# Performance work log

Measured on AMD Instinct MI355X. Metric: run time of the kernel, lower is better.

The kernel has to match this reference:

```python
import jax, jax.numpy as jnp
import numpy as np

B, T, S, D = 8, 512, 512, 1024
NUM_HEADS = 16
REUSE_HEADS = 8
NEW_HEADS = NUM_HEADS - REUSE_HEADS
KEY_DIM = 64
VALUE_DIM = 64
PE_MAX = 512  # pe_max_seq_length


def setup_inputs() -> dict:
    key = jax.random.key(0)
    ks = jax.random.split(key, 12)
    s = 0.02
    return {
        "query": jax.random.normal(ks[0], (B, T, D), jnp.float32),
        "value": jax.random.normal(ks[1], (B, S, D), jnp.float32),
        # scores reused from a previous layer (already softmaxed there)
        "reuse_attention_scores": jax.random.uniform(ks[2], (B, REUSE_HEADS, T, S), jnp.float32),
        "Wq": jax.random.normal(ks[3], (D, NEW_HEADS, KEY_DIM), jnp.float32) * s,
        "bq": jnp.zeros((NEW_HEADS, KEY_DIM), jnp.float32),
        "Wk": jax.random.normal(ks[4], (D, NEW_HEADS, KEY_DIM), jnp.float32) * s,
        "bk": jnp.zeros((NEW_HEADS, KEY_DIM), jnp.float32),
        "Wv": jax.random.normal(ks[5], (D, NUM_HEADS, VALUE_DIM), jnp.float32) * s,
        "bv": jnp.zeros((NUM_HEADS, VALUE_DIM), jnp.float32),
        # relative position embeddings: [1, new_heads, 2*PE_MAX - 1]
        "pos_emb": jax.random.truncated_normal(ks[6], -2.0, 2.0, (1, NEW_HEADS, 2 * PE_MAX - 1), jnp.float32) * 0.2,
        # output denses: one for reused heads (no bias), one for new heads (bias)
        "Wo_reuse": jax.random.normal(ks[7], (REUSE_HEADS, VALUE_DIM, D), jnp.float32) * s,
        "Wo_new": jax.random.normal(ks[8], (NEW_HEADS, VALUE_DIM, D), jnp.float32) * s,
        "bo": jnp.zeros((D,), jnp.float32),
    }


def reference(query, value, reuse_attention_scores, Wq, bq, Wk, bk, Wv, bv,
              pos_emb, Wo_reuse, Wo_new, bo):
    # projections (EinsumDense abc,cde->abde + bias over last two dims)
    q = jnp.einsum("btd,dnh->btnh", query, Wq) + bq           # [B,T,Hn,kd]
    k = jnp.einsum("bsd,dnh->bsnh", value, Wk) + bk           # [B,S,Hn,kd]
    v = jnp.einsum("bsd,dnh->bsnh", value, Wv) + bv           # [B,S,H,vd]
    v_reuse, v_new = v[:, :, :REUSE_HEADS, :], v[:, :, REUSE_HEADS:, :]

    # new-head scores: scaled QK^T  (dot_product_equation 'aecd,abcd->acbe')
    q = q * (1.0 / np.sqrt(float(KEY_DIM)))
    new_scores = jnp.einsum("bsnh,btnh->bnts", k, q)          # [B,Hn,T,S]

    # relative position bias: index = clip(key_pos - query_pos + PE_MAX-1)
    rel = jnp.arange(S)[None, :] - jnp.arange(T)[:, None] + (PE_MAX - 1)
    rel = jnp.clip(rel, 0, 2 * PE_MAX - 2)                    # [T,S]
    bias = pos_emb[0][:, rel]                                 # [Hn,T,S]
    new_scores = jax.nn.softmax(new_scores + bias[None], axis=-1)

    # reused heads consume previous-layer scores directly (dropout=0)
    reuse_scores = reuse_attention_scores[:, :REUSE_HEADS]
    out_reuse = jnp.einsum("bnts,bsnh->btnh", reuse_scores, v_reuse)
    out_new = jnp.einsum("bnts,bsnh->btnh", new_scores, v_new)

    # separate output projections, summed; bias only on the new-heads dense
    out = (jnp.einsum("btnh,nhd->btd", out_reuse, Wo_reuse)
           + jnp.einsum("btnh,nhd->btd", out_new, Wo_new) + bo)
    return out
```

## Files before the change

### kernel.cpp

```cpp
#include <hip/hip_runtime.h>
#include <hip/hip_bf16.h>

typedef __bf16 bf16_t;
typedef __bf16 bf16x8 __attribute__((ext_vector_type(8)));
typedef float  f32x4  __attribute__((ext_vector_type(4)));

#define GLDS(gsrc, ldst)                                                              \
  __builtin_amdgcn_global_load_lds(                                                   \
      (const __attribute__((address_space(1))) unsigned int*)(gsrc),                  \
      (__attribute__((address_space(3))) unsigned int*)(ldst), 16, 0, 0)

__global__ void k_convert2(const float* __restrict__ a, bf16_t* __restrict__ da,
                           const float* __restrict__ b, bf16_t* __restrict__ db, int n8) {
  int i = blockIdx.x * blockDim.x + threadIdx.x;
  const float* s; bf16_t* d;
  if (i < n8) { s = a; d = da; } else { s = b; d = db; i -= n8; }
  const float4* p = reinterpret_cast<const float4*>(s) + 2 * (long)i;
  float4 x = p[0], y = p[1];
  bf16x8 o;
  o[0] = (bf16_t)x.x; o[1] = (bf16_t)x.y; o[2] = (bf16_t)x.z; o[3] = (bf16_t)x.w;
  o[4] = (bf16_t)y.x; o[5] = (bf16_t)y.y; o[6] = (bf16_t)y.z; o[7] = (bf16_t)y.w;
  reinterpret_cast<bf16x8*>(d)[i] = o;
}

struct TArgs {
  const float* src[5];
  bf16_t* dst[5];
  int C[5], Ct[5], off[5], blk0[6];
  float scale[5];
};
__global__ void k_transpose5(TArgs ta) {
  __shared__ float tile[32][33];
  const int bid = blockIdx.x;
  int s = 0;
  while (bid >= ta.blk0[s + 1]) ++s;
  const int bi = bid - ta.blk0[s];
  const int Ct = ta.Ct[s];
  const int c0 = (bi % Ct) * 32, r0 = (bi / Ct) * 32;
  const int C = ta.C[s];
  const float* src = ta.src[s];
  const int lx = threadIdx.x & 31, ly = threadIdx.x >> 5;
  #pragma unroll
  for (int i = 0; i < 32; i += 8)
    tile[ly + i][lx] = src[(long)(r0 + ly + i) * C + (c0 + lx)];
  __syncthreads();
  const float sc = ta.scale[s];
  bf16_t* dst = ta.dst[s];
  const int off = ta.off[s];
  #pragma unroll
  for (int i = 0; i < 32; i += 8)
    dst[(long)(c0 + ly + i) * 1024 + off + (r0 + lx)] = (bf16_t)(tile[lx][ly + i] * sc);
}

struct ProjItem {
  const bf16_t* A; const bf16_t* B; bf16_t* C; const float* bias;
  float bscale; int ldc; int writeT;
};
struct ProjArgs { ProjItem it[3]; };

__global__ __launch_bounds__(256)
void k_gemm_proj(ProjArgs pa) {
  __shared__ char smem[18432];
  bf16_t* lsA = (bf16_t*)smem;
  bf16_t* lsB = (bf16_t*)(smem + 8192);

  const int bid = blockIdx.x;
  const int z = bid < 128 ? 0 : (bid < 256 ? 1 : 2);
  const int local = bid - (z == 0 ? 0 : (z == 1 ? 128 : 256));
  const ProjItem it = pa.it[z];
  const int t = threadIdx.x, lane = t & 63, wid = t >> 6;
  const int wr = wid >> 1, wc = wid & 1;
  const int m0 = (local & 31) * 128, n0 = (local >> 5) * 128;
  const int lhi = lane >> 4, llo = lane & 15;

  const bf16_t* Ab = it.A + (long)m0 * 1024;
  const bf16_t* Bb = it.B + (long)n0 * 1024;

  const int e0 = t * 8,        r0s = e0 >> 5, c0s = e0 & 31;
  const int e1 = (256 + t) * 8, r1s = e1 >> 5, c1s = e1 & 31;
  bf16_t* lA0 = lsA + wid * 512;
  bf16_t* lA1 = lsA + 2048 + wid * 512;
  bf16_t* lB0 = lsB + wid * 512;
  bf16_t* lB1 = lsB + 2048 + wid * 512;

  f32x4 acc[4][4] = {};

  for (int k0 = 0; k0 < 1024; k0 += 32) {
    GLDS(Ab + (long)r0s * 1024 + k0 + c0s, lA0);
    GLDS(Ab + (long)r1s * 1024 + k0 + c1s, lA1);
    GLDS(Bb + (long)r0s * 1024 + k0 + c0s, lB0);
    GLDS(Bb + (long)r1s * 1024 + k0 + c1s, lB1);
    __syncthreads();
    bf16x8 a[4], b[4];
    #pragma unroll
    for (int mi = 0; mi < 4; ++mi)
      a[mi] = *reinterpret_cast<const bf16x8*>(lsA + (wr * 64 + mi * 16 + llo) * 32 + lhi * 8);
    #pragma unroll
    for (int ni = 0; ni < 4; ++ni)
      b[ni] = *reinterpret_cast<const bf16x8*>(lsB + (wc * 64 + ni * 16 + llo) * 32 + lhi * 8);
    #pragma unroll
    for (int mi = 0; mi < 4; ++mi)
      #pragma unroll
      for (int ni = 0; ni < 4; ++ni)
        acc[mi][ni] = __builtin_amdgcn_mfma_f32_16x16x32_bf16(a[mi], b[ni], acc[mi][ni], 0, 0, 0);
    __syncthreads();
  }

  #pragma unroll
  for (int mi = 0; mi < 4; ++mi)
    #pragma unroll
    for (int ni = 0; ni < 4; ++ni) {
      const float bv = it.bias[n0 + wc * 64 + ni * 16 + llo] * it.bscale;
      #pragma unroll
      for (int r = 0; r < 4; ++r) acc[mi][ni][r] += bv;
    }

  if (!it.writeT) {
    bf16_t* E = (bf16_t*)smem;
    #pragma unroll
    for (int p = 0; p < 2; ++p) {
      if (wr == p) {
        #pragma unroll
        for (int mi = 0; mi < 4; ++mi)
          #pragma unroll
          for (int ni = 0; ni < 4; ++ni)
            #pragma unroll
            for (int r = 0; r < 4; ++r)
              E[(mi * 16 + lhi * 4 + r) * 136 + wc * 64 + ni * 16 + llo] = (bf16_t)acc[mi][ni][r];
      }
      __syncthreads();
      #pragma unroll
      for (int round = 0; round < 4; ++round) {
        const int row = (t >> 4) + round * 16;
        const int l16 = t & 15;
        float4 v = *reinterpret_cast<const float4*>((char*)E + row * 272 + l16 * 16);
        *reinterpret_cast<float4*>(it.C + (long)(m0 + p * 64 + row) * it.ldc + n0 + l16 * 8) = v;
      }
      __syncthreads();
    }
  } else {
    bf16_t* E = (bf16_t*)smem;
    #pragma unroll
    for (int p = 0; p < 2; ++p) {
      if (wr == p) {
        #pragma unroll
        for (int mi = 0; mi < 4; ++mi)
          #pragma unroll
          for (int ni = 0; ni < 4; ++ni)
            #pragma unroll
            for (int r = 0; r < 4; ++r)
              E[(wc * 64 + ni * 16 + llo) * 72 + mi * 16 + lhi * 4 + r] = (bf16_t)acc[mi][ni][r];
      }
      __syncthreads();
      #pragma unroll
      for (int round = 0; round < 4; ++round) {
        const int nr = (t >> 3) + round * 32;
        const int l8 = t & 7;
        float4 v = *reinterpret_cast<const float4*>((char*)E + nr * 144 + l8 * 16);
        *reinterpret_cast<float4*>(it.C + (long)(n0 + nr) * it.ldc + m0 + p * 64 + l8 * 8) = v;
      }
      __syncthreads();
    }
  }
}

__global__ __launch_bounds__(256)
void k_gemm_out(const bf16_t* __restrict__ A_, const bf16_t* __restrict__ B_,
                float* __restrict__ C_, const float* __restrict__ bias) {
  __shared__ char smem[16896];
  bf16_t* lsA = (bf16_t*)smem;
  bf16_t* lsB = (bf16_t*)(smem + 4096);

  const int t = threadIdx.x, lane = t & 63, wid = t >> 6;
  const int wr = wid >> 1, wc = wid & 1;
  const int m0 = blockIdx.x * 64, n0 = blockIdx.y * 128;
  const int lhi = lane >> 4, llo = lane & 15;

  const bf16_t* Ab = A_ + (long)m0 * 1024;
  const bf16_t* Bb = B_ + (long)n0 * 1024;

  const int e0 = t * 8,        r0s = e0 >> 5, c0s = e0 & 31;
  const int e1 = (256 + t) * 8, r1s = e1 >> 5, c1s = e1 & 31;
  bf16_t* lA0 = lsA + wid * 512;
  bf16_t* lB0 = lsB + wid * 512;
  bf16_t* lB1 = lsB + 2048 + wid * 512;

  f32x4 acc[2][4] = {};

  for (int k0 = 0; k0 < 1024; k0 += 32) {
    GLDS(Ab + (long)r0s * 1024 + k0 + c0s, lA0);
    GLDS(Bb + (long)r0s * 1024 + k0 + c0s, lB0);
    GLDS(Bb + (long)r1s * 1024 + k0 + c1s, lB1);
    __syncthreads();
    bf16x8 a[2], b[4];
    #pragma unroll
    for (int mi = 0; mi < 2; ++mi)
      a[mi] = *reinterpret_cast<const bf16x8*>(lsA + (wr * 32 + mi * 16 + llo) * 32 + lhi * 8);
    #pragma unroll
    for (int ni = 0; ni < 4; ++ni)
      b[ni] = *reinterpret_cast<const bf16x8*>(lsB + (wc * 64 + ni * 16 + llo) * 32 + lhi * 8);
    #pragma unroll
    for (int mi = 0; mi < 2; ++mi)
      #pragma unroll
      for (int ni = 0; ni < 4; ++ni)
        acc[mi][ni] = __builtin_amdgcn_mfma_f32_16x16x32_bf16(a[mi], b[ni], acc[mi][ni], 0, 0, 0);
    __syncthreads();
  }

  #pragma unroll
  for (int mi = 0; mi < 2; ++mi)
    #pragma unroll
    for (int ni = 0; ni < 4; ++ni) {
      const float bv = bias[n0 + wc * 64 + ni * 16 + llo];
      #pragma unroll
      for (int r = 0; r < 4; ++r) acc[mi][ni][r] += bv;
    }

  float* E = (float*)smem;
  #pragma unroll
  for (int p = 0; p < 2; ++p) {
    if (wr == p) {
      #pragma unroll
      for (int mi = 0; mi < 2; ++mi)
        #pragma unroll
        for (int ni = 0; ni < 4; ++ni)
          #pragma unroll
          for (int r = 0; r < 4; ++r)
            E[(mi * 16 + lhi * 4 + r) * 132 + wc * 64 + ni * 16 + llo] = acc[mi][ni][r];
    }
    __syncthreads();
    #pragma unroll
    for (int round = 0; round < 4; ++round) {
      const int row = (t >> 5) + round * 8;
      const int l32 = t & 31;
      float4 v = *reinterpret_cast<const float4*>((char*)E + row * 528 + l32 * 16);
      *reinterpret_cast<float4*>(C_ + (long)(m0 + p * 32 + row) * 1024 + n0 + l32 * 4) = v;
    }
    __syncthreads();
  }
}

__global__ __launch_bounds__(256, 2)
void k_fattn(const bf16_t* __restrict__ qb, const bf16_t* __restrict__ kb,
             const bf16_t* __restrict__ vbT, const float* __restrict__ pe,
             bf16_t* __restrict__ om) {
  __shared__ float pes[1024];
  __shared__ bf16_t Kt[128 * 64];
  __shared__ bf16_t Vt[64 * 128];
  __shared__ bf16_t Pt[4][16 * 128];

  const int bid = blockIdx.x;
  const int tt = bid >> 6;
  const int bh = bid & 63;
  const int b = bh >> 3, h = bh & 7;
  const int lane = threadIdx.x & 63, w = threadIdx.x >> 6;
  const int lhi = lane >> 4, llo = lane & 15;
  const int t0w = tt * 64 + w * 16;

  char* KtB = (char*)Kt;
  char* VtB = (char*)Vt;
  char* PtB = (char*)Pt + w * 4096;

  const bf16_t* Ksrc = kb + (long)(b * 512) * 512 + h * 64;
  const bf16_t* Vsrc = vbT + (long)(512 + h * 64) * 4096 + b * 512;
  const int krow = w * 32 + (lane >> 3);
  const int kcol = ((lane & 7) ^ (lane >> 3)) << 3;
  const int vn   = w * 16 + (lane >> 4);
  bf16_t* kdst = (bf16_t*)(KtB + w * 4096);
  bf16_t* vdst = (bf16_t*)(VtB + w * 4096);

#define STAGE_K(it_)                                                                   \
  { _Pragma("unroll")                                                                  \
    for (int g = 0; g < 4; ++g)                                                        \
      GLDS(Ksrc + (long)((it_) * 128 + krow + g * 8) * 512 + kcol, kdst + g * 512); }
#define STAGE_V(it_)                                                                   \
  { _Pragma("unroll")                                                                  \
    for (int g = 0; g < 4; ++g)                                                        \
      GLDS(Vsrc + (long)(vn + g * 4) * 4096 + (it_) * 128 +                            \
               (((lane & 15) ^ (g * 4 + (lane >> 4))) << 3),                           \
           vdst + g * 512); }

  STAGE_K(0);
  STAGE_V(0);

  const bf16_t* Qb = qb + (long)(b * 512 + t0w + llo) * 512 + h * 64;
  bf16x8 qf0 = *reinterpret_cast<const bf16x8*>(Qb + lhi * 8);
  bf16x8 qf1 = *reinterpret_cast<const bf16x8*>(Qb + 32 + lhi * 8);
  for (int i = threadIdx.x; i < 1023; i += 256) pes[i] = pe[h * 1023 + i];

  f32x4 oacc[4] = {};
  float lr[4] = {0.f, 0.f, 0.f, 0.f};

  __syncthreads();

  for (int it = 0; it < 4; ++it) {
    const int s0 = it * 128;

    f32x4 acc[8] = {};
    #pragma unroll
    for (int st = 0; st < 8; ++st) {
      const int rowb = st * 16 + llo;
      const int sw = (rowb & 7) << 4;
      bf16x8 kf0 = *reinterpret_cast<const bf16x8*>(KtB + rowb * 128 + ((lhi * 16) ^ sw));
      bf16x8 kf1 = *reinterpret_cast<const bf16x8*>(KtB + rowb * 128 + ((64 + lhi * 16) ^ sw));
      acc[st] = __builtin_amdgcn_mfma_f32_16x16x32_bf16(qf0, kf0, acc[st], 0, 0, 0);
      acc[st] = __builtin_amdgcn_mfma_f32_16x16x32_bf16(qf1, kf1, acc[st], 0, 0, 0);
    }

    __syncthreads();
    if (it < 3) STAGE_K(it + 1);

    #pragma unroll
    for (int r = 0; r < 4; ++r) {
      const int tl = lhi * 4 + r;
      const int bidx = s0 + llo - (t0w + tl) + 511;
      const int swp = (tl & 15) << 4;
      float lp = 0.f;
      #pragma unroll
      for (int st = 0; st < 8; ++st) {
        const float e = __expf(acc[st][r] + pes[bidx + st * 16]);
        lp += e;
        *reinterpret_cast<bf16_t*>(PtB + tl * 256 + (((st * 16 + llo) * 2) ^ swp)) = (bf16_t)e;
      }
      lr[r] += lp;
    }

    const int swa = llo << 4;
    #pragma unroll
    for (int ks = 0; ks < 4; ++ks) {
      bf16x8 pa = *reinterpret_cast<const bf16x8*>(PtB + llo * 256 + ((ks * 64 + lhi * 16) ^ swa));
      #pragma unroll
      for (int ni = 0; ni < 4; ++ni) {
        const int rowv = ni * 16 + llo;
        bf16x8 vf = *reinterpret_cast<const bf16x8*>(VtB + rowv * 256 + ((ks * 64 + lhi * 16) ^ swa));
        oacc[ni] = __builtin_amdgcn_mfma_f32_16x16x32_bf16(pa, vf, oacc[ni], 0, 0, 0);
      }
    }

    __syncthreads();
    if (it < 3) STAGE_V(it + 1);
  }

  #pragma unroll
  for (int r = 0; r < 4; ++r) {
    lr[r] += __shfl_xor(lr[r], 1);
    lr[r] += __shfl_xor(lr[r], 2);
    lr[r] += __shfl_xor(lr[r], 4);
    lr[r] += __shfl_xor(lr[r], 8);
  }

  bf16_t* Ew = (bf16_t*)PtB;
  #pragma unroll
  for (int ni = 0; ni < 4; ++ni)
    #pragma unroll
    for (int r = 0; r < 4; ++r)
      Ew[(lhi * 4 + r) * 72 + ni * 16 + llo] = (bf16_t)(oacc[ni][r] * (1.f / lr[r]));
  #pragma unroll
  for (int round = 0; round < 2; ++round) {
    const int lr8 = (lane >> 3) + round * 8;
    const int l8 = lane & 7;
    float4 v = *reinterpret_cast<const float4*>((char*)Ew + lr8 * 144 + l8 * 16);
    *reinterpret_cast<float4*>(om + (long)(b * 512 + t0w + lr8) * 1024 + 512 + h * 64 + l8 * 8) = v;
  }
#undef STAGE_K
#undef STAGE_V
}

__global__ __launch_bounds__(256, 3)
void k_pvr(const float* __restrict__ reuse, const bf16_t* __restrict__ vbT,
           bf16_t* __restrict__ om) {
  __shared__ float red[2][32][68];
  const int z = blockIdx.y;
  const int b = z >> 3, head = z & 7;
  const int lane = threadIdx.x & 63, w = threadIdx.x >> 6;
  const int lhi = lane >> 4, llo = lane & 15;
  const int m0 = blockIdx.x * 32;
  const int ks0 = w * 128;

  const float*  Af = reuse + (long)b * 2097152 + (long)head * 262144;
  const bf16_t* Bp = vbT + (long)(head * 64) * 4096 + b * 512;

  f32x4 acc[2][4] = {};
  float4 Ax[2][2][2];
  bf16x8 Bx[2][4];

  #define PV_LOAD(kq, buf)                                                              \
    {                                                                                   \
      const int kk = ks0 + (kq) * 32 + lhi * 8;                                         \
      _Pragma("unroll")                                                                 \
      for (int mi = 0; mi < 2; ++mi) {                                                  \
        const float4* p = reinterpret_cast<const float4*>(Af + (long)(m0 + mi * 16 + llo) * 512 + kk); \
        Ax[buf][mi][0] = p[0];                                                          \
        Ax[buf][mi][1] = p[1];                                                          \
      }                                                                                 \
      _Pragma("unroll")                                                                 \
      for (int ni = 0; ni < 4; ++ni)                                                    \
        Bx[buf][ni] = *reinterpret_cast<const bf16x8*>(Bp + (long)(ni * 16 + llo) * 4096 + kk); \
    }

  PV_LOAD(0, 0);
  #pragma unroll
  for (int kq = 0; kq < 4; ++kq) {
    const int cb = kq & 1;
    if (kq < 3) {
      const int nb = (kq + 1) & 1;
      PV_LOAD(kq + 1, nb);
    }
    bf16x8 a[2];
    #pragma unroll
    for (int mi = 0; mi < 2; ++mi) {
      float4 x = Ax[cb][mi][0], y = Ax[cb][mi][1];
      bf16x8 tv;
      tv[0] = (bf16_t)x.x; tv[1] = (bf16_t)x.y; tv[2] = (bf16_t)x.z; tv[3] = (bf16_t)x.w;
      tv[4] = (bf16_t)y.x; tv[5] = (bf16_t)y.y; tv[6] = (bf16_t)y.z; tv[7] = (bf16_t)y.w;
      a[mi] = tv;
    }
    #pragma unroll
    for (int mi = 0; mi < 2; ++mi)
      #pragma unroll
      for (int ni = 0; ni < 4; ++ni)
        acc[mi][ni] = __builtin_amdgcn_mfma_f32_16x16x32_bf16(a[mi], Bx[cb][ni], acc[mi][ni], 0, 0, 0);
  }
  #undef PV_LOAD

  if (w >= 2) {
    #pragma unroll
    for (int mi = 0; mi < 2; ++mi)
      #pragma unroll
      for (int ni = 0; ni < 4; ++ni)
        #pragma unroll
        for (int r = 0; r < 4; ++r)
          red[w - 2][mi * 16 + lhi * 4 + r][ni * 16 + llo] = acc[mi][ni][r];
  }
  __syncthreads();
  if (w < 2) {
    #pragma unroll
    for (int mi = 0; mi < 2; ++mi)
      #pragma unroll
      for (int ni = 0; ni < 4; ++ni)
        #pragma unroll
        for (int r = 0; r < 4; ++r)
          acc[mi][ni][r] += red[w][mi * 16 + lhi * 4 + r][ni * 16 + llo];
  }
  __syncthreads();
  if (w == 1) {
    #pragma unroll
    for (int mi = 0; mi < 2; ++mi)
      #pragma unroll
      for (int ni = 0; ni < 4; ++ni)
        #pragma unroll
        for (int r = 0; r < 4; ++r)
          red[0][mi * 16 + lhi * 4 + r][ni * 16 + llo] = acc[mi][ni][r];
  }
  __syncthreads();
  if (w == 0) {
    bf16_t* E = (bf16_t*)&red[1][0][0];
    #pragma unroll
    for (int mi = 0; mi < 2; ++mi)
      #pragma unroll
      for (int ni = 0; ni < 4; ++ni)
        #pragma unroll
        for (int r = 0; r < 4; ++r) {
          const int mr = mi * 16 + lhi * 4 + r;
          const int nn = ni * 16 + llo;
          E[mr * 72 + nn] = (bf16_t)(acc[mi][ni][r] + red[0][mr][nn]);
        }
    bf16_t* Cb = om + (long)b * 524288 + head * 64;
    #pragma unroll
    for (int round = 0; round < 4; ++round) {
      const int row = (lane >> 3) + round * 8;
      const int l8 = lane & 7;
      float4 v = *reinterpret_cast<const float4*>((char*)E + row * 144 + l8 * 16);
      *reinterpret_cast<float4*>(Cb + (long)(m0 + row) * 1024 + l8 * 8) = v;
    }
  }
}

extern "C" void kernel_launch(void* const* d_in, const int* in_sizes, int n_in,
                              void* d_out, int out_size, void* d_ws, size_t ws_size,
                              hipStream_t stream) {
  const float* query = (const float*)d_in[0];
  const float* value = (const float*)d_in[1];
  const float* reuse = (const float*)d_in[2];
  const float* Wq    = (const float*)d_in[3];
  const float* bq    = (const float*)d_in[4];
  const float* Wk    = (const float*)d_in[5];
  const float* bk    = (const float*)d_in[6];
  const float* Wv    = (const float*)d_in[7];
  const float* bv    = (const float*)d_in[8];
  const float* pe    = (const float*)d_in[9];
  const float* WoR   = (const float*)d_in[10];
  const float* WoN   = (const float*)d_in[11];
  const float* bo    = (const float*)d_in[12];
  float* out = (float*)d_out;
  (void)in_sizes; (void)n_in; (void)out_size; (void)ws_size;

  char* w = (char*)d_ws;
  bf16_t* qx  = (bf16_t*)(w);
  bf16_t* vx  = (bf16_t*)(w + (8L  << 20));
  bf16_t* WqT = (bf16_t*)(w + (16L << 20));
  bf16_t* WkT = (bf16_t*)(w + (17L << 20));
  bf16_t* WvT = (bf16_t*)(w + (18L << 20));
  bf16_t* WoT = (bf16_t*)(w + (20L << 20));
  bf16_t* qb  = (bf16_t*)(w + (22L << 20));
  bf16_t* kb  = (bf16_t*)(w + (26L << 20));
  bf16_t* vbT = (bf16_t*)(w + (30L << 20));
  bf16_t* om  = (bf16_t*)(w + (38L << 20));

  k_convert2<<<4096, 256, 0, stream>>>(query, qx, value, vx, 524288);

  TArgs ta;
  ta.src[0] = Wq;  ta.dst[0] = WqT; ta.C[0] = 512;  ta.Ct[0] = 16; ta.off[0] = 0;   ta.scale[0] = 0.125f;
  ta.src[1] = Wk;  ta.dst[1] = WkT; ta.C[1] = 512;  ta.Ct[1] = 16; ta.off[1] = 0;   ta.scale[1] = 1.f;
  ta.src[2] = Wv;  ta.dst[2] = WvT; ta.C[2] = 1024; ta.Ct[2] = 32; ta.off[2] = 0;   ta.scale[2] = 1.f;
  ta.src[3] = WoR; ta.dst[3] = WoT; ta.C[3] = 1024; ta.Ct[3] = 32; ta.off[3] = 0;   ta.scale[3] = 1.f;
  ta.src[4] = WoN; ta.dst[4] = WoT; ta.C[4] = 1024; ta.Ct[4] = 32; ta.off[4] = 512; ta.scale[4] = 1.f;
  ta.blk0[0] = 0; ta.blk0[1] = 512; ta.blk0[2] = 1024; ta.blk0[3] = 2048; ta.blk0[4] = 2560; ta.blk0[5] = 3072;
  k_transpose5<<<3072, 256, 0, stream>>>(ta);

  ProjArgs pa;
  pa.it[0] = { qx, WqT, qb,  bq, 0.125f, 512,  0 };
  pa.it[1] = { vx, WkT, kb,  bk, 1.f,    512,  0 };
  pa.it[2] = { vx, WvT, vbT, bv, 1.f,    4096, 1 };
  k_gemm_proj<<<dim3(512), 256, 0, stream>>>(pa);

  k_fattn<<<dim3(512), 256, 0, stream>>>(qb, kb, vbT, pe, om);

  k_pvr<<<dim3(16, 64), 256, 0, stream>>>(reuse, vbT, om);

  k_gemm_out<<<dim3(64, 8), 256, 0, stream>>>(om, WoT, out, bo);
}
```

Baseline: 99.35 us.

## Merge launches and double-buffer LDS in projection and output GEMMs

The conversion and weight-transpose kernels are merged into one launch, and the new-head flash attention and reuse-head PV kernels are merged into a single grid that branches on block index. The two GEMMs now double-buffer their LDS tiles, issuing the next k-slice's global-to-LDS loads before the MFMAs on the current slice. This aims to remove launch gaps and tail idling between small kernels and to hide global load latency in the GEMMs. In exchange it uses more shared memory per block, which may lower occupancy, and the merged attention kernel sets launch bounds of 3 blocks per CU where the flash path previously used 2, which may add register pressure.

```diff
diff --git a/kernel.cpp b/kernel.cpp
--- a/kernel.cpp
+++ b/kernel.cpp
@@ -9,19 +9,6 @@
   __builtin_amdgcn_global_load_lds(                                                   \
       (const __attribute__((address_space(1))) unsigned int*)(gsrc),                  \
       (__attribute__((address_space(3))) unsigned int*)(ldst), 16, 0, 0)
-
-__global__ void k_convert2(const float* __restrict__ a, bf16_t* __restrict__ da,
-                           const float* __restrict__ b, bf16_t* __restrict__ db, int n8) {
-  int i = blockIdx.x * blockDim.x + threadIdx.x;
-  const float* s; bf16_t* d;
-  if (i < n8) { s = a; d = da; } else { s = b; d = db; i -= n8; }
-  const float4* p = reinterpret_cast<const float4*>(s) + 2 * (long)i;
-  float4 x = p[0], y = p[1];
-  bf16x8 o;
-  o[0] = (bf16_t)x.x; o[1] = (bf16_t)x.y; o[2] = (bf16_t)x.z; o[3] = (bf16_t)x.w;
-  o[4] = (bf16_t)y.x; o[5] = (bf16_t)y.y; o[6] = (bf16_t)y.z; o[7] = (bf16_t)y.w;
-  reinterpret_cast<bf16x8*>(d)[i] = o;
-}
 
 struct TArgs {
   const float* src[5];
@@ -29,12 +16,31 @@
   int C[5], Ct[5], off[5], blk0[6];
   float scale[5];
 };
-__global__ void k_transpose5(TArgs ta) {
+struct CTArgs {
+  const float* qa; bf16_t* qd;
+  const float* va; bf16_t* vd;
+  TArgs ta;
+};
+__global__ void k_convtrans(CTArgs ca) {
   __shared__ float tile[32][33];
   const int bid = blockIdx.x;
+  if (bid < 4096) {
+    int i = bid * 256 + threadIdx.x;
+    const float* s; bf16_t* d;
+    if (i < 524288) { s = ca.qa; d = ca.qd; } else { s = ca.va; d = ca.vd; i -= 524288; }
+    const float4* p = reinterpret_cast<const float4*>(s) + 2 * (long)i;
+    float4 x = p[0], y = p[1];
+    bf16x8 o;
+    o[0] = (bf16_t)x.x; o[1] = (bf16_t)x.y; o[2] = (bf16_t)x.z; o[3] = (bf16_t)x.w;
+    o[4] = (bf16_t)y.x; o[5] = (bf16_t)y.y; o[6] = (bf16_t)y.z; o[7] = (bf16_t)y.w;
+    reinterpret_cast<bf16x8*>(d)[i] = o;
+    return;
+  }
+  const TArgs& ta = ca.ta;
+  const int tb = bid - 4096;
   int s = 0;
-  while (bid >= ta.blk0[s + 1]) ++s;
-  const int bi = bid - ta.blk0[s];
+  while (tb >= ta.blk0[s + 1]) ++s;
+  const int bi = tb - ta.blk0[s];
   const int Ct = ta.Ct[s];
   const int c0 = (bi % Ct) * 32, r0 = (bi / Ct) * 32;
   const int C = ta.C[s];
@@ -60,10 +66,7 @@
 
 __global__ __launch_bounds__(256)
 void k_gemm_proj(ProjArgs pa) {
-  __shared__ char smem[18432];
-  bf16_t* lsA = (bf16_t*)smem;
-  bf16_t* lsB = (bf16_t*)(smem + 8192);
-
+  __shared__ char smem[32768];
   const int bid = blockIdx.x;
   const int z = bid < 128 ? 0 : (bid < 256 ? 1 : 2);
   const int local = bid - (z == 0 ? 0 : (z == 1 ? 128 : 256));
@@ -78,33 +81,39 @@
 
   const int e0 = t * 8,        r0s = e0 >> 5, c0s = e0 & 31;
   const int e1 = (256 + t) * 8, r1s = e1 >> 5, c1s = e1 & 31;
-  bf16_t* lA0 = lsA + wid * 512;
-  bf16_t* lA1 = lsA + 2048 + wid * 512;
-  bf16_t* lB0 = lsB + wid * 512;
-  bf16_t* lB1 = lsB + 2048 + wid * 512;
+
+#define PSTAGE(k0_, bsel)                                                     \
+  { bf16_t* bA = (bf16_t*)(smem + (bsel) * 16384);                            \
+    bf16_t* bB = (bf16_t*)(smem + (bsel) * 16384 + 8192);                     \
+    GLDS(Ab + (long)r0s * 1024 + (k0_) + c0s, bA + wid * 512);                \
+    GLDS(Ab + (long)r1s * 1024 + (k0_) + c1s, bA + 2048 + wid * 512);         \
+    GLDS(Bb + (long)r0s * 1024 + (k0_) + c0s, bB + wid * 512);                \
+    GLDS(Bb + (long)r1s * 1024 + (k0_) + c1s, bB + 2048 + wid * 512); }
 
   f32x4 acc[4][4] = {};
-
-  for (int k0 = 0; k0 < 1024; k0 += 32) {
-    GLDS(Ab + (long)r0s * 1024 + k0 + c0s, lA0);
-    GLDS(Ab + (long)r1s * 1024 + k0 + c1s, lA1);
-    GLDS(Bb + (long)r0s * 1024 + k0 + c0s, lB0);
-    GLDS(Bb + (long)r1s * 1024 + k0 + c1s, lB1);
-    __syncthreads();
+  PSTAGE(0, 0);
+  __syncthreads();
+  int cur = 0;
+  for (int t32 = 0; t32 < 32; ++t32) {
+    bf16_t* sA = (bf16_t*)(smem + cur * 16384);
+    bf16_t* sB = (bf16_t*)(smem + cur * 16384 + 8192);
     bf16x8 a[4], b[4];
     #pragma unroll
     for (int mi = 0; mi < 4; ++mi)
-      a[mi] = *reinterpret_cast<const bf16x8*>(lsA + (wr * 64 + mi * 16 + llo) * 32 + lhi * 8);
+      a[mi] = *reinterpret_cast<const bf16x8*>(sA + (wr * 64 + mi * 16 + llo) * 32 + lhi * 8);
     #pragma unroll
     for (int ni = 0; ni < 4; ++ni)
-      b[ni] = *reinterpret_cast<const bf16x8*>(lsB + (wc * 64 + ni * 16 + llo) * 32 + lhi * 8);
+      b[ni] = *reinterpret_cast<const bf16x8*>(sB + (wc * 64 + ni * 16 + llo) * 32 + lhi * 8);
+    if (t32 < 31) PSTAGE((t32 + 1) * 32, cur ^ 1);
     #pragma unroll
     for (int mi = 0; mi < 4; ++mi)
       #pragma unroll
       for (int ni = 0; ni < 4; ++ni)
         acc[mi][ni] = __builtin_amdgcn_mfma_f32_16x16x32_bf16(a[mi], b[ni], acc[mi][ni], 0, 0, 0);
     __syncthreads();
-  }
+    cur ^= 1;
+  }
+#undef PSTAGE
 
   #pragma unroll
   for (int mi = 0; mi < 4; ++mi)
@@ -167,10 +176,7 @@
 __global__ __launch_bounds__(256)
 void k_gemm_out(const bf16_t* __restrict__ A_, const bf16_t* __restrict__ B_,
                 float* __restrict__ C_, const float* __restrict__ bias) {
-  __shared__ char smem[16896];
-  bf16_t* lsA = (bf16_t*)smem;
-  bf16_t* lsB = (bf16_t*)(smem + 4096);
-
+  __shared__ char smem[24576];
   const int t = threadIdx.x, lane = t & 63, wid = t >> 6;
   const int wr = wid >> 1, wc = wid & 1;
   const int m0 = blockIdx.x * 64, n0 = blockIdx.y * 128;
@@ -181,31 +187,38 @@
 
   const int e0 = t * 8,        r0s = e0 >> 5, c0s = e0 & 31;
   const int e1 = (256 + t) * 8, r1s = e1 >> 5, c1s = e1 & 31;
-  bf16_t* lA0 = lsA + wid * 512;
-  bf16_t* lB0 = lsB + wid * 512;
-  bf16_t* lB1 = lsB + 2048 + wid * 512;
+
+#define OSTAGE(k0_, bsel)                                                     \
+  { bf16_t* bA = (bf16_t*)(smem + (bsel) * 12288);                            \
+    bf16_t* bB = (bf16_t*)(smem + (bsel) * 12288 + 4096);                     \
+    GLDS(Ab + (long)r0s * 1024 + (k0_) + c0s, bA + wid * 512);                \
+    GLDS(Bb + (long)r0s * 1024 + (k0_) + c0s, bB + wid * 512);                \
+    GLDS(Bb + (long)r1s * 1024 + (k0_) + c1s, bB + 2048 + wid * 512); }
 
   f32x4 acc[2][4] = {};
-
-  for (int k0 = 0; k0 < 1024; k0 += 32) {
-    GLDS(Ab + (long)r0s * 1024 + k0 + c0s, lA0);
-    GLDS(Bb + (long)r0s * 1024 + k0 + c0s, lB0);
-    GLDS(Bb + (long)r1s * 1024 + k0 + c1s, lB1);
-    __syncthreads();
+  OSTAGE(0, 0);
+  __syncthreads();
+  int cur = 0;
+  for (int t32 = 0; t32 < 32; ++t32) {
+    bf16_t* sA = (bf16_t*)(smem + cur * 12288);
+    bf16_t* sB = (bf16_t*)(smem + cur * 12288 + 4096);
     bf16x8 a[2], b[4];
     #pragma unroll
     for (int mi = 0; mi < 2; ++mi)
-      a[mi] = *reinterpret_cast<const bf16x8*>(lsA + (wr * 32 + mi * 16 + llo) * 32 + lhi * 8);
+      a[mi] = *reinterpret_cast<const bf16x8*>(sA + (wr * 32 + mi * 16 + llo) * 32 + lhi * 8);
     #pragma unroll
     for (int ni = 0; ni < 4; ++ni)
-      b[ni] = *reinterpret_cast<const bf16x8*>(lsB + (wc * 64 + ni * 16 + llo) * 32 + lhi * 8);
+      b[ni] = *reinterpret_cast<const bf16x8*>(sB + (wc * 64 + ni * 16 + llo) * 32 + lhi * 8);
+    if (t32 < 31) OSTAGE((t32 + 1) * 32, cur ^ 1);
     #pragma unroll
     for (int mi = 0; mi < 2; ++mi)
       #pragma unroll
       for (int ni = 0; ni < 4; ++ni)
         acc[mi][ni] = __builtin_amdgcn_mfma_f32_16x16x32_bf16(a[mi], b[ni], acc[mi][ni], 0, 0, 0);
     __syncthreads();
-  }
+    cur ^= 1;
+  }
+#undef OSTAGE
 
   #pragma unroll
   for (int mi = 0; mi < 2; ++mi)
@@ -240,34 +253,33 @@
   }
 }
 
-__global__ __launch_bounds__(256, 2)
-void k_fattn(const bf16_t* __restrict__ qb, const bf16_t* __restrict__ kb,
-             const bf16_t* __restrict__ vbT, const float* __restrict__ pe,
-             bf16_t* __restrict__ om) {
-  __shared__ float pes[1024];
-  __shared__ bf16_t Kt[128 * 64];
-  __shared__ bf16_t Vt[64 * 128];
-  __shared__ bf16_t Pt[4][16 * 128];
-
+__global__ __launch_bounds__(256, 3)
+void k_attn_all(const bf16_t* __restrict__ qb, const bf16_t* __restrict__ kb,
+                const bf16_t* __restrict__ vbT, const float* __restrict__ pe,
+                const float* __restrict__ reuse, bf16_t* __restrict__ om) {
+  __shared__ char smem[53248];
   const int bid = blockIdx.x;
-  const int tt = bid >> 6;
-  const int bh = bid & 63;
-  const int b = bh >> 3, h = bh & 7;
   const int lane = threadIdx.x & 63, w = threadIdx.x >> 6;
   const int lhi = lane >> 4, llo = lane & 15;
-  const int t0w = tt * 64 + w * 16;
-
-  char* KtB = (char*)Kt;
-  char* VtB = (char*)Vt;
-  char* PtB = (char*)Pt + w * 4096;
-
-  const bf16_t* Ksrc = kb + (long)(b * 512) * 512 + h * 64;
-  const bf16_t* Vsrc = vbT + (long)(512 + h * 64) * 4096 + b * 512;
-  const int krow = w * 32 + (lane >> 3);
-  const int kcol = ((lane & 7) ^ (lane >> 3)) << 3;
-  const int vn   = w * 16 + (lane >> 4);
-  bf16_t* kdst = (bf16_t*)(KtB + w * 4096);
-  bf16_t* vdst = (bf16_t*)(VtB + w * 4096);
+
+  if (bid < 512) {
+    float* pes = (float*)smem;
+    char* KtB = smem + 4096;
+    char* VtB = smem + 4096 + 16384;
+    char* PtB = smem + 4096 + 32768 + w * 4096;
+
+    const int tt = bid >> 6;
+    const int bh = bid & 63;
+    const int b = bh >> 3, h = bh & 7;
+    const int t0w = tt * 64 + w * 16;
+
+    const bf16_t* Ksrc = kb + (long)(b * 512) * 512 + h * 64;
+    const bf16_t* Vsrc = vbT + (long)(512 + h * 64) * 4096 + b * 512;
+    const int krow = w * 32 + (lane >> 3);
+    const int kcol = ((lane & 7) ^ (lane >> 3)) << 3;
+    const int vn   = w * 16 + (lane >> 4);
+    bf16_t* kdst = (bf16_t*)(KtB + w * 4096);
+    bf16_t* vdst = (bf16_t*)(VtB + w * 4096);
 
 #define STAGE_K(it_)                                                                   \
   { _Pragma("unroll")                                                                  \
@@ -280,101 +292,99 @@
                (((lane & 15) ^ (g * 4 + (lane >> 4))) << 3),                           \
            vdst + g * 512); }
 
-  STAGE_K(0);
-  STAGE_V(0);
-
-  const bf16_t* Qb = qb + (long)(b * 512 + t0w + llo) * 512 + h * 64;
-  bf16x8 qf0 = *reinterpret_cast<const bf16x8*>(Qb + lhi * 8);
-  bf16x8 qf1 = *reinterpret_cast<const bf16x8*>(Qb + 32 + lhi * 8);
-  for (int i = threadIdx.x; i < 1023; i += 256) pes[i] = pe[h * 1023 + i];
-
-  f32x4 oacc[4] = {};
-  float lr[4] = {0.f, 0.f, 0.f, 0.f};
-
-  __syncthreads();
-
-  for (int it = 0; it < 4; ++it) {
-    const int s0 = it * 128;
-
-    f32x4 acc[8] = {};
-    #pragma unroll
-    for (int st = 0; st < 8; ++st) {
-      const int rowb = st * 16 + llo;
-      const int sw = (rowb & 7) << 4;
-      bf16x8 kf0 = *reinterpret_cast<const bf16x8*>(KtB + rowb * 128 + ((lhi * 16) ^ sw));
-      bf16x8 kf1 = *reinterpret_cast<const bf16x8*>(KtB + rowb * 128 + ((64 + lhi * 16) ^ sw));
-      acc[st] = __builtin_amdgcn_mfma_f32_16x16x32_bf16(qf0, kf0, acc[st], 0, 0, 0);
-      acc[st] = __builtin_amdgcn_mfma_f32_16x16x32_bf16(qf1, kf1, acc[st], 0, 0, 0);
-    }
+    STAGE_K(0);
+    STAGE_V(0);
+
+    const bf16_t* Qb = qb + (long)(b * 512 + t0w + llo) * 512 + h * 64;
+    bf16x8 qf0 = *reinterpret_cast<const bf16x8*>(Qb + lhi * 8);
+    bf16x8 qf1 = *reinterpret_cast<const bf16x8*>(Qb + 32 + lhi * 8);
+    for (int i = threadIdx.x; i < 1023; i += 256) pes[i] = pe[h * 1023 + i];
+
+    f32x4 oacc[4] = {};
+    float lr[4] = {0.f, 0.f, 0.f, 0.f};
 
     __syncthreads();
-    if (it < 3) STAGE_K(it + 1);
+
+    for (int it = 0; it < 4; ++it) {
+      const int s0 = it * 128;
+
+      f32x4 acc[8] = {};
+      #pragma unroll
+      for (int st = 0; st < 8; ++st) {
+        const int rowb = st * 16 + llo;
+        const int sw = (rowb & 7) << 4;
+        bf16x8 kf0 = *reinterpret_cast<const bf16x8*>(KtB + rowb * 128 + ((lhi * 16) ^ sw));
+        bf16x8 kf1 = *reinterpret_cast<const bf16x8*>(KtB + rowb * 128 + ((64 + lhi * 16) ^ sw));
+        acc[st] = __builtin_amdgcn_mfma_f32_16x16x32_bf16(qf0, kf0, acc[st], 0, 0, 0);
+        acc[st] = __builtin_amdgcn_mfma_f32_16x16x32_bf16(qf1, kf1, acc[st], 0, 0, 0);
+      }
+
+      __syncthreads();
+      if (it < 3) STAGE_K(it + 1);
+
+      #pragma unroll
+      for (int r = 0; r < 4; ++r) {
+        const int tl = lhi * 4 + r;
+        const int bidx = s0 + llo - (t0w + tl) + 511;
+        const int swp = (tl & 15) << 4;
+        float lp = 0.f;
+        #pragma unroll
+        for (int st = 0; st < 8; ++st) {
+          const float e = __expf(acc[st][r] + pes[bidx + st * 16]);
+          lp += e;
+          *reinterpret_cast<bf16_t*>(PtB + tl * 256 + (((st * 16 + llo) * 2) ^ swp)) = (bf16_t)e;
+        }
+        lr[r] += lp;
+      }
+
+      const int swa = llo << 4;
+      #pragma unroll
+      for (int ks = 0; ks < 4; ++ks) {
+        bf16x8 pav = *reinterpret_cast<const bf16x8*>(PtB + llo * 256 + ((ks * 64 + lhi * 16) ^ swa));
+        #pragma unroll
+        for (int ni = 0; ni < 4; ++ni) {
+          const int rowv = ni * 16 + llo;
+          bf16x8 vf = *reinterpret_cast<const bf16x8*>(VtB + rowv * 256 + ((ks * 64 + lhi * 16) ^ swa));
+          oacc[ni] = __builtin_amdgcn_mfma_f32_16x16x32_bf16(pav, vf, oacc[ni], 0, 0, 0);
+        }
+      }
+
+      __syncthreads();
+      if (it < 3) STAGE_V(it + 1);
+    }
 
     #pragma unroll
     for (int r = 0; r < 4; ++r) {
-      const int tl = lhi * 4 + r;
-      const int bidx = s0 + llo - (t0w + tl) + 511;
-      const int swp = (tl & 15) << 4;
-      float lp = 0.f;
-      #pragma unroll
-      for (int st = 0; st < 8; ++st) {
-        const float e = __expf(acc[st][r] + pes[bidx + st * 16]);
-        lp += e;
-        *reinterpret_cast<bf16_t*>(PtB + tl * 256 + (((st * 16 + llo) * 2) ^ swp)) = (bf16_t)e;
-      }
-      lr[r] += lp;
-    }
-
-    const int swa = llo << 4;
-    #pragma unroll
-    for (int ks = 0; ks < 4; ++ks) {
-      bf16x8 pa = *reinterpret_cast<const bf16x8*>(PtB + llo * 256 + ((ks * 64 + lhi * 16) ^ swa));
-      #pragma unroll
-      for (int ni = 0; ni < 4; ++ni) {
-        const int rowv = ni * 16 + llo;
-        bf16x8 vf = *reinterpret_cast<const bf16x8*>(VtB + rowv * 256 + ((ks * 64 + lhi * 16) ^ swa));
-        oacc[ni] = __builtin_amdgcn_mfma_f32_16x16x32_bf16(pa, vf, oacc[ni], 0, 0, 0);
-      }
-    }
-
-    __syncthreads();
-    if (it < 3) STAGE_V(it + 1);
-  }
-
-  #pragma unroll
-  for (int r = 0; r < 4; ++r) {
-    lr[r] += __shfl_xor(lr[r], 1);
-    lr[r] += __shfl_xor(lr[r], 2);
-    lr[r] += __shfl_xor(lr[r], 4);
-    lr[r] += __shfl_xor(lr[r], 8);
-  }
-
-  bf16_t* Ew = (bf16_t*)PtB;
-  #pragma unroll
-  for (int ni = 0; ni < 4; ++ni)
-    #pragma unroll
-    for (int r = 0; r < 4; ++r)
-      Ew[(lhi * 4 + r) * 72 + ni * 16 + llo] = (bf16_t)(oacc[ni][r] * (1.f / lr[r]));
-  #pragma unroll
-  for (int round = 0; round < 2; ++round) {
-    const int lr8 = (lane >> 3) + round * 8;
-    const int l8 = lane & 7;
-    float4 v = *reinterpret_cast<const float4*>((char*)Ew + lr8 * 144 + l8 * 16);
-    *reinterpret_cast<float4*>(om + (long)(b * 512 + t0w + lr8) * 1024 + 512 + h * 64 + l8 * 8) = v;
-  }
+      lr[r] += __shfl_xor(lr[r], 1);
+      lr[r] += __shfl_xor(lr[r], 2);
+      lr[r] += __shfl_xor(lr[r], 4);
+      lr[r] += __shfl_xor(lr[r], 8);
+    }
+
+    bf16_t* Ew = (bf16_t*)PtB;
+    #pragma unroll
+    for (int ni = 0; ni < 4; ++ni)
+      #pragma unroll
+      for (int r = 0; r < 4; ++r)
+        Ew[(lhi * 4 + r) * 72 + ni * 16 + llo] = (bf16_t)(oacc[ni][r] * (1.f / lr[r]));
+    #pragma unroll
+    for (int round = 0; round < 2; ++round) {
+      const int lr8 = (lane >> 3) + round * 8;
+      const int l8 = lane & 7;
+      float4 v = *reinterpret_cast<const float4*>((char*)Ew + lr8 * 144 + l8 * 16);
+      *reinterpret_cast<float4*>(om + (long)(b * 512 + t0w + lr8) * 1024 + 512 + h * 64 + l8 * 8) = v;
+    }
 #undef STAGE_K
 #undef STAGE_V
-}
-
-__global__ __launch_bounds__(256, 3)
-void k_pvr(const float* __restrict__ reuse, const bf16_t* __restrict__ vbT,
-           bf16_t* __restrict__ om) {
-  __shared__ float red[2][32][68];
-  const int z = blockIdx.y;
-  const int b = z >> 3, head = z & 7;
-  const int lane = threadIdx.x & 63, w = threadIdx.x >> 6;
-  const int lhi = lane >> 4, llo = lane & 15;
-  const int m0 = blockIdx.x * 32;
+    return;
+  }
+
+  typedef float RedRow[32][68];
+  RedRow* red = (RedRow*)smem;
+  const int pid = bid - 512;
+  const int bh = pid >> 4;
+  const int b = bh >> 3, head = bh & 7;
+  const int m0 = (pid & 15) * 32;
   const int ks0 = w * 128;
 
   const float*  Af = reuse + (long)b * 2097152 + (long)head * 262144;
@@ -507,16 +517,15 @@
   bf16_t* vbT = (bf16_t*)(w + (30L << 20));
   bf16_t* om  = (bf16_t*)(w + (38L << 20));
 
-  k_convert2<<<4096, 256, 0, stream>>>(query, qx, value, vx, 524288);
-
-  TArgs ta;
-  ta.src[0] = Wq;  ta.dst[0] = WqT; ta.C[0] = 512;  ta.Ct[0] = 16; ta.off[0] = 0;   ta.scale[0] = 0.125f;
-  ta.src[1] = Wk;  ta.dst[1] = WkT; ta.C[1] = 512;  ta.Ct[1] = 16; ta.off[1] = 0;   ta.scale[1] = 1.f;
-  ta.src[2] = Wv;  ta.dst[2] = WvT; ta.C[2] = 1024; ta.Ct[2] = 32; ta.off[2] = 0;   ta.scale[2] = 1.f;
-  ta.src[3] = WoR; ta.dst[3] = WoT; ta.C[3] = 1024; ta.Ct[3] = 32; ta.off[3] = 0;   ta.scale[3] = 1.f;
-  ta.src[4] = WoN; ta.dst[4] = WoT; ta.C[4] = 1024; ta.Ct[4] = 32; ta.off[4] = 512; ta.scale[4] = 1.f;
-  ta.blk0[0] = 0; ta.blk0[1] = 512; ta.blk0[2] = 1024; ta.blk0[3] = 2048; ta.blk0[4] = 2560; ta.blk0[5] = 3072;
-  k_transpose5<<<3072, 256, 0, stream>>>(ta);
+  CTArgs ca;
+  ca.qa = query; ca.qd = qx; ca.va = value; ca.vd = vx;
+  ca.ta.src[0] = Wq;  ca.ta.dst[0] = WqT; ca.ta.C[0] = 512;  ca.ta.Ct[0] = 16; ca.ta.off[0] = 0;   ca.ta.scale[0] = 0.125f;
+  ca.ta.src[1] = Wk;  ca.ta.dst[1] = WkT; ca.ta.C[1] = 512;  ca.ta.Ct[1] = 16; ca.ta.off[1] = 0;   ca.ta.scale[1] = 1.f;
+  ca.ta.src[2] = Wv;  ca.ta.dst[2] = WvT; ca.ta.C[2] = 1024; ca.ta.Ct[2] = 32; ca.ta.off[2] = 0;   ca.ta.scale[2] = 1.f;
+  ca.ta.src[3] = WoR; ca.ta.dst[3] = WoT; ca.ta.C[3] = 1024; ca.ta.Ct[3] = 32; ca.ta.off[3] = 0;   ca.ta.scale[3] = 1.f;
+  ca.ta.src[4] = WoN; ca.ta.dst[4] = WoT; ca.ta.C[4] = 1024; ca.ta.Ct[4] = 32; ca.ta.off[4] = 512; ca.ta.scale[4] = 1.f;
+  ca.ta.blk0[0] = 0; ca.ta.blk0[1] = 512; ca.ta.blk0[2] = 1024; ca.ta.blk0[3] = 2048; ca.ta.blk0[4] = 2560; ca.ta.blk0[5] = 3072;
+  k_convtrans<<<dim3(7168), 256, 0, stream>>>(ca);
 
   ProjArgs pa;
   pa.it[0] = { qx, WqT, qb,  bq, 0.125f, 512,  0 };
@@ -524,9 +533,7 @@
   pa.it[2] = { vx, WvT, vbT, bv, 1.f,    4096, 1 };
   k_gemm_proj<<<dim3(512), 256, 0, stream>>>(pa);
 
-  k_fattn<<<dim3(512), 256, 0, stream>>>(qb, kb, vbT, pe, om);
-
-  k_pvr<<<dim3(16, 64), 256, 0, stream>>>(reuse, vbT, om);
+  k_attn_all<<<dim3(1536), 256, 0, stream>>>(qb, kb, vbT, pe, reuse, om);
 
   k_gemm_out<<<dim3(64, 8), 256, 0, stream>>>(om, WoT, out, bo);
 }
```

After: 90.53 us. 8.9% less time.
